# Kernel optimization log

Hardware: AMD Instinct MI355X
Metric: run time of the kernel (lower is better)

The kernel has to match this reference:

```python
import jax, jax.numpy as jnp
import numpy as np

WORD = 512
ED = 64


def setup_inputs() -> dict:
    key = jax.random.key(0)
    ks = jax.random.split(key, 7)
    x = jax.random.normal(ks[0], (4, 4096, WORD), dtype=jnp.float32)
    # Dense layer params (kernel + bias) for query/key/value projections
    s = 1.0 / np.sqrt(WORD)
    Wq = jax.random.normal(ks[1], (WORD, ED), dtype=jnp.float32) * s
    Wk = jax.random.normal(ks[2], (WORD, ED), dtype=jnp.float32) * s
    Wv = jax.random.normal(ks[3], (WORD, ED), dtype=jnp.float32) * s
    bq = jnp.zeros((ED,), dtype=jnp.float32)
    bk = jnp.zeros((ED,), dtype=jnp.float32)
    bv = jnp.zeros((ED,), dtype=jnp.float32)
    return {"x": x, "Wq": Wq, "bq": bq, "Wk": Wk, "bk": bk, "Wv": Wv, "bv": bv}


def reference(x, Wq, bq, Wk, bk, Wv, bv):
    # Q, K, V: [B, S, ED]
    Q = jnp.einsum('bsw,we->bse', x, Wq) + bq
    K = jnp.einsum('bsw,we->bse', x, Wk) + bk
    V = jnp.einsum('bsw,we->bse', x, Wv) + bv
    scale = 1.0 / jnp.sqrt(jnp.float32(ED))
    score = jnp.einsum('bqe,bke->bqk', Q, K) * scale  # [B, S, S]
    attn = jax.nn.softmax(score, axis=-1)
    Z = jnp.einsum('bqk,bke->bqe', attn, V)  # [B, S, ED]
    return Z
```

## Files before the change

### kernel.cpp

```cpp
#include <hip/hip_runtime.h>
#include <cstdint>


typedef __bf16 bf16x8 __attribute__((ext_vector_type(8)));
typedef float f32x4 __attribute__((ext_vector_type(4)));
typedef float f32x16 __attribute__((ext_vector_type(16)));
typedef int i32x2 __attribute__((ext_vector_type(2)));

#define SCALEQ 0.18033688011112042f

#define WT_OFF 0u
#define Q_OFF  262144u
#define KV_OFF 2359296u
#define L_OFF  6553600u
#define OP_OFF 7077888u

#if defined(__has_builtin)
#if __has_builtin(__builtin_amdgcn_permlane32_swap)
#define HAVE_PLSWAP 1
#endif
#if __has_builtin(__builtin_amdgcn_global_load_lds)
#define HAVE_GLL 1
#endif
#endif
#ifndef HAVE_PLSWAP
#define HAVE_PLSWAP 0
#endif
#ifndef HAVE_GLL
#define HAVE_GLL 0
#endif

__device__ __forceinline__ unsigned short bf16_1(float a) {
  unsigned ua = __builtin_bit_cast(unsigned, a);
  ua += 0x7FFFu + ((ua >> 16) & 1u);
  return (unsigned short)(ua >> 16);
}
__device__ __forceinline__ unsigned pk_bf16(float a, float b) {
  unsigned ua = __builtin_bit_cast(unsigned, a);
  unsigned ub = __builtin_bit_cast(unsigned, b);
  ua += 0x7FFFu + ((ua >> 16) & 1u);
  ub += 0x7FFFu + ((ub >> 16) & 1u);
  return (ua >> 16) | (ub & 0xFFFF0000u);
}
__device__ __forceinline__ unsigned pkru(float lo, float hi) {
  unsigned a = __builtin_bit_cast(unsigned, lo) + 0x8000u;
  unsigned b = __builtin_bit_cast(unsigned, hi) + 0x8000u;
  return __builtin_amdgcn_perm(b, a, 0x07060302u);
}
__device__ __forceinline__ void plswap(unsigned& x, unsigned& y, unsigned hl) {
#if HAVE_PLSWAP
  i32x2 r = __builtin_amdgcn_permlane32_swap((int)x, (int)y, false, false);
  x = (unsigned)r[0];
  y = (unsigned)r[1];
#else
  unsigned xs = (unsigned)__shfl_xor((int)x, 32);
  unsigned ys = (unsigned)__shfl_xor((int)y, 32);
  unsigned nx = hl ? ys : x;
  unsigned ny = hl ? y : xs;
  x = nx;
  y = ny;
#endif
}
#if HAVE_GLL
__device__ __forceinline__ void gll16(const void* g, void* l) {
  __builtin_amdgcn_global_load_lds(
      (const __attribute__((address_space(1))) void*)g,
      (__attribute__((address_space(3))) void*)l, 16, 0, 0);
}
#endif

__global__ __launch_bounds__(256) void prep_w(const float* __restrict__ Wq,
                                              const float* __restrict__ Wk,
                                              const float* __restrict__ Wv,
                                              unsigned short* __restrict__ wt2) {
  unsigned gtid = blockIdx.x * 256u + threadIdx.x;
  unsigned mat = gtid >> 15, rem = gtid & 32767u;
  const float* w = (mat == 0) ? Wq : (mat == 1) ? Wk : Wv;
  float v = w[rem];
  unsigned k = rem >> 6, n = rem & 63u;
  unsigned col = mat * 64u + n;
  unsigned ntg = col >> 4, l15c = col & 15u;
  unsigned kc = k >> 5, quad = (k >> 3) & 3u, j = k & 7u;
  wt2[((ntg * 16u + kc) * 64u + quad * 16u + l15c) * 8u + j] = bf16_1(v);
}

__global__ __launch_bounds__(256, 4) void qkv_proj(
    const float* __restrict__ x, const unsigned short* __restrict__ wt2,
    const float* __restrict__ bq, const float* __restrict__ bk,
    const float* __restrict__ bv, unsigned short* __restrict__ qws,
    unsigned short* __restrict__ kvws) {
  __shared__ __align__(16) char xs[16384];
  __shared__ float biasl[192];
  const unsigned t = threadIdx.x;
  const unsigned row0 = blockIdx.x * 16u;
  const unsigned w = t >> 6, lane = t & 63u, l15 = lane & 15u, quad = lane >> 4;

  if (t < 192u) {
    unsigned mat = t >> 6, n = t & 63u;
    biasl[t] = (mat == 0) ? bq[n] : (mat == 1) ? bk[n] : bv[n];
  }
#pragma unroll
  for (int i = 0; i < 8; i++) {
    unsigned idx4 = t + 256u * (unsigned)i;
    unsigned fidx = idx4 * 4u;
    unsigned row = fidx >> 9, k = fidx & 511u, g = k >> 3;
    float4 f = *(const float4*)(x + row0 * 512u + fidx);
    int2 v = make_int2(pkru(f.x, f.y), pkru(f.z, f.w));
    *(int2*)(xs + row * 1024u + ((g ^ (row & 7u)) << 4) + (k & 7u) * 2u) = v;
  }
  __syncthreads();

  f32x4 acc[3];
#pragma unroll
  for (int i = 0; i < 3; i++) acc[i] = {0.f, 0.f, 0.f, 0.f};
  const unsigned arow = l15;
  const unsigned short* wbase = wt2 + (w * 3u * 1024u + lane) * 8u;

  int4 cur[3], nxt[3];
#pragma unroll
  for (int nt = 0; nt < 3; nt++)
    cur[nt] = *(const int4*)(wbase + (unsigned)nt * 8192u);
  for (unsigned kc = 0; kc < 16u; kc++) {
    if (kc < 15u) {
#pragma unroll
      for (int nt = 0; nt < 3; nt++)
        nxt[nt] = *(const int4*)(wbase + ((unsigned)nt * 16u + kc + 1u) * 512u);
    }
    unsigned ag = kc * 4u + quad;
    int4 av = *(const int4*)(xs + arow * 1024u + ((ag ^ (arow & 7u)) << 4));
    bf16x8 a = __builtin_bit_cast(bf16x8, av);
#pragma unroll
    for (int nt = 0; nt < 3; nt++)
      acc[nt] = __builtin_amdgcn_mfma_f32_16x16x32_bf16(
          a, __builtin_bit_cast(bf16x8, cur[nt]), acc[nt], 0, 0, 0);
#pragma unroll
    for (int nt = 0; nt < 3; nt++) cur[nt] = nxt[nt];
  }
  unsigned sb = row0 + quad * 4u;
#pragma unroll
  for (int nt = 0; nt < 3; nt++) {
    unsigned col = w * 48u + (unsigned)nt * 16u + l15;
    unsigned mat = col >> 6, n = col & 63u;
    float bb = biasl[col];
    if (mat == 0) {
#pragma unroll
      for (int r = 0; r < 4; r++)
        qws[(sb + (unsigned)r) * 64u + n] = bf16_1((acc[nt][r] + bb) * SCALEQ);
    } else if (mat == 1) {
#pragma unroll
      for (int r = 0; r < 4; r++) {
        unsigned s = sb + (unsigned)r;
        unsigned bb2 = s >> 12, tile = (s & 4095u) >> 6, kap = s & 63u;
        kvws[(bb2 * 64u + tile) * 8192u + (n >> 3) * 512u + kap * 8u + (n & 7u)] =
            bf16_1(acc[nt][r] + bb);
      }
    } else {
      unsigned s = sb;
      unsigned bb2 = s >> 12, tile = (s & 4095u) >> 6;
      unsigned kg = (s & 63u) >> 3, j0 = s & 7u;
      int2 pv = make_int2(pk_bf16(acc[nt][0] + bb, acc[nt][1] + bb),
                          pk_bf16(acc[nt][2] + bb, acc[nt][3] + bb));
      *(int2*)(kvws + (bb2 * 64u + tile) * 8192u + (8u + kg) * 512u + n * 8u +
               j0) = pv;
    }
  }
}

__global__ __launch_bounds__(256, 3) void attn(
    const unsigned short* __restrict__ qws,
    const unsigned short* __restrict__ kvws, float* __restrict__ lws,
    unsigned short* __restrict__ opp) {
  __shared__ __align__(16) char sm[34816];
  const unsigned t = threadIdx.x;
  const unsigned w = t >> 6, lane = t & 63u, l31 = lane & 31u, hl = lane >> 5;
  const unsigned bid = blockIdx.x;
  const unsigned ks = bid >> 7;
  const unsigned b = (bid >> 5) & 3u;
  const unsigned qt = bid & 31u;
  const unsigned q0 = qt * 128u + w * 32u;
  const unsigned short* kvb = kvws + (b * 64u + ks * 8u) * 8192u + lane * 8u;

  bf16x8 qf[4];
#pragma unroll
  for (int kq = 0; kq < 4; kq++)
    qf[kq] = __builtin_bit_cast(
        bf16x8, *(const int4*)(qws + (b * 4096u + q0 + l31) * 64u +
                               (unsigned)kq * 16u + hl * 8u));
  f32x16 accO[2];
#pragma unroll
  for (int dh = 0; dh < 2; dh++)
#pragma unroll
    for (int r = 0; r < 16; r++) accO[dh][r] = 0.f;
  float lsum = 0.f;

#if HAVE_GLL
#define STAGE(kt_, bi_)                                                \
  {                                                                    \
    _Pragma("unroll") for (int i = 0; i < 4; i++) {                    \
      unsigned c = (unsigned)i * 4u + w;                               \
      gll16(kvb + (kt_)*8192u + c * 512u, sm + (bi_)*16384u + c * 1024u); \
    }                                                                  \
  }
  STAGE(0u, 0u);
  __syncthreads();
#else
  int4 stg[4];
#define LOADT(kt_)                                                         \
  {                                                                        \
    _Pragma("unroll") for (int i = 0; i < 4; i++) stg[i] =                 \
        *(const int4*)(kvb + (kt_)*8192u + ((unsigned)i * 4u + w) * 512u); \
  }
  LOADT(0u);
  {
#pragma unroll
    for (int i = 0; i < 4; i++)
      *(int4*)(sm + ((unsigned)i * 4u + w) * 1024u + lane * 16u) = stg[i];
  }
  __syncthreads();
#endif

  for (unsigned kt = 0; kt < 8u; kt++) {
    char* kb = sm + (kt & 1u) * 16384u;
    int4 kfr[8], vfr[8];
#pragma unroll
    for (int kq = 0; kq < 4; kq++)
#pragma unroll
      for (int kh = 0; kh < 2; kh++)
        kfr[kq * 2 + kh] = *(const int4*)(
            kb + (((unsigned)kq * 2u + hl) * 64u + (unsigned)kh * 32u + l31) * 16u);
#pragma unroll
    for (int kqg = 0; kqg < 4; kqg++)
#pragma unroll
      for (int dh = 0; dh < 2; dh++)
        vfr[kqg * 2 + dh] = *(const int4*)(
            kb + 8192u +
            (((unsigned)kqg * 2u + hl) * 64u + (unsigned)dh * 32u + l31) * 16u);
#if HAVE_GLL
    if (kt < 7u) STAGE(kt + 1u, (kt + 1u) & 1u);
#else
    if (kt < 7u) LOADT(kt + 1u);
#endif
#pragma unroll
    for (int kh = 0; kh < 2; kh++) {
      f32x16 z;
#pragma unroll
      for (int r = 0; r < 16; r++) z[r] = 0.f;
#pragma unroll
      for (int kq = 0; kq < 4; kq++)
        z = __builtin_amdgcn_mfma_f32_32x32x16_bf16(
            __builtin_bit_cast(bf16x8, kfr[kq * 2 + kh]), qf[kq], z, 0, 0, 0);
      float lp = 0.f;
#pragma unroll
      for (int r = 0; r < 16; r++) {
        z[r] = __builtin_amdgcn_exp2f(z[r]);
        lp += z[r];
      }
      lsum += lp;
      unsigned pk8[8];
#pragma unroll
      for (int c2 = 0; c2 < 4; c2++) {
        pk8[2 * c2] = pkru(z[4 * c2 + 0], z[4 * c2 + 1]);
        pk8[2 * c2 + 1] = pkru(z[4 * c2 + 2], z[4 * c2 + 3]);
      }
#pragma unroll
      for (int kqpl = 0; kqpl < 2; kqpl++) {
        unsigned a0 = pk8[4 * kqpl + 0], a1 = pk8[4 * kqpl + 1];
        unsigned b0 = pk8[4 * kqpl + 2], b1 = pk8[4 * kqpl + 3];
        plswap(a0, b0, hl);
        plswap(a1, b1, hl);
        int4 fr = make_int4((int)a0, (int)a1, (int)b0, (int)b1);
        bf16x8 pf = __builtin_bit_cast(bf16x8, fr);
        unsigned kqg = (unsigned)kh * 2u + (unsigned)kqpl;
#pragma unroll
        for (int dh = 0; dh < 2; dh++)
          accO[dh] = __builtin_amdgcn_mfma_f32_32x32x16_bf16(
              __builtin_bit_cast(bf16x8, vfr[kqg * 2u + (unsigned)dh]), pf,
              accO[dh], 0, 0, 0);
      }
    }
    __syncthreads();
#if !HAVE_GLL
    if (kt < 7u) {
#pragma unroll
      for (int i = 0; i < 4; i++)
        *(int4*)(sm + ((kt + 1u) & 1u) * 16384u +
                 ((unsigned)i * 4u + w) * 1024u + lane * 16u) = stg[i];
      __syncthreads();
    }
#endif
  }
  float lt = lsum + __shfl_xor(lsum, 32);
  if (hl == 0u) lws[ks * 16384u + b * 4096u + q0 + l31] = lt;
  float* sc = (float*)(sm + w * 8704u);
#pragma unroll
  for (int dh = 0; dh < 2; dh++)
#pragma unroll
    for (int r = 0; r < 16; r++) {
      unsigned d = (unsigned)dh * 32u + (unsigned)(r & 3) +
                   8u * (unsigned)(r >> 2) + 4u * hl;
      sc[l31 * 68u + d] = accO[dh][r];
    }
#pragma unroll
  for (int i = 0; i < 4; i++) {
    unsigned ql = (lane >> 3) + (unsigned)i * 8u;
    unsigned d0 = (lane & 7u) * 8u;
    float4 f0 = *(const float4*)(sc + ql * 68u + d0);
    float4 f1 = *(const float4*)(sc + ql * 68u + d0 + 4u);
    int4 pv = make_int4(pkru(f0.x, f0.y), pkru(f0.z, f0.w),
                        pkru(f1.x, f1.y), pkru(f1.z, f1.w));
    *(int4*)(opp + ks * 1048576u + (b * 4096u + q0 + ql) * 64u + d0) = pv;
  }
}

__global__ __launch_bounds__(256) void combine(const unsigned short* __restrict__ opp,
                                               const float* __restrict__ lws,
                                               float* __restrict__ out) {
#pragma unroll
  for (int ii = 0; ii < 2; ii++) {
    unsigned slot = blockIdx.x * 512u + threadIdx.x + 256u * (unsigned)ii;
    unsigned q = slot >> 4, c = (slot & 15u) * 4u;
    float l = 0.f;
#pragma unroll
    for (int s = 0; s < 8; s++) l += lws[(unsigned)s * 16384u + q];
    float inv = 1.0f / l;
    float4 r = make_float4(0.f, 0.f, 0.f, 0.f);
#pragma unroll
    for (int s = 0; s < 8; s++) {
      int2 pv = *(const int2*)(opp + (unsigned)s * 1048576u + q * 64u + c);
      r.x += __builtin_bit_cast(float, (unsigned)pv.x << 16);
      r.y += __builtin_bit_cast(float, (unsigned)pv.x & 0xFFFF0000u);
      r.z += __builtin_bit_cast(float, (unsigned)pv.y << 16);
      r.w += __builtin_bit_cast(float, (unsigned)pv.y & 0xFFFF0000u);
    }
    r.x *= inv; r.y *= inv; r.z *= inv; r.w *= inv;
    *(float4*)(out + q * 64u + c) = r;
  }
}

extern "C" void kernel_launch(void* const* d_in, const int* in_sizes, int n_in,
                              void* d_out, int out_size, void* d_ws,
                              size_t ws_size, hipStream_t stream) {
  const float* x = (const float*)d_in[0];
  const float* Wq = (const float*)d_in[1];
  const float* bq = (const float*)d_in[2];
  const float* Wk = (const float*)d_in[3];
  const float* bk = (const float*)d_in[4];
  const float* Wv = (const float*)d_in[5];
  const float* bv = (const float*)d_in[6];
  char* ws = (char*)d_ws;
  unsigned short* wt2 = (unsigned short*)(ws + WT_OFF);
  unsigned short* qb = (unsigned short*)(ws + Q_OFF);
  unsigned short* kvb = (unsigned short*)(ws + KV_OFF);
  float* lp = (float*)(ws + L_OFF);
  unsigned short* opp = (unsigned short*)(ws + OP_OFF);
  float* outp = (float*)d_out;

  prep_w<<<384, 256, 0, stream>>>(Wq, Wk, Wv, wt2);
  qkv_proj<<<1024, 256, 0, stream>>>(x, wt2, bq, bk, bv, qb, kvb);
  attn<<<1024, 256, 0, stream>>>(qb, kvb, lp, opp);
  combine<<<512, 256, 0, stream>>>(opp, lp, outp);
}
```

Before: 122.4 us.

## Rebalance attention key split to six chunks, double qkv rows per block, use cvt_pk_bf16

The attention kernel now splits keys into 6 uneven chunks (10-11 tiles each) instead of 8, giving 768 blocks rather than 1024 so the grid fits resident slots better and less partial output goes through combine. The QKV projection handles 32 rows per block so each weight fragment load feeds two MFMAs. Manual bf16 rounding is replaced with the hardware v_cvt_pk_bf16_f32 instruction, the exp-sum becomes a tree reduction, and s_setprio raises wave priority around the MFMA section. The trade-off is more work per attention block and uneven chunk sizes. It also uses more LDS in the projection kernel, which can lower occupancy.

```diff
diff --git a/kernel.cpp b/kernel.cpp
--- a/kernel.cpp
+++ b/kernel.cpp
@@ -35,17 +35,10 @@
   ua += 0x7FFFu + ((ua >> 16) & 1u);
   return (unsigned short)(ua >> 16);
 }
-__device__ __forceinline__ unsigned pk_bf16(float a, float b) {
-  unsigned ua = __builtin_bit_cast(unsigned, a);
-  unsigned ub = __builtin_bit_cast(unsigned, b);
-  ua += 0x7FFFu + ((ua >> 16) & 1u);
-  ub += 0x7FFFu + ((ub >> 16) & 1u);
-  return (ua >> 16) | (ub & 0xFFFF0000u);
-}
-__device__ __forceinline__ unsigned pkru(float lo, float hi) {
-  unsigned a = __builtin_bit_cast(unsigned, lo) + 0x8000u;
-  unsigned b = __builtin_bit_cast(unsigned, hi) + 0x8000u;
-  return __builtin_amdgcn_perm(b, a, 0x07060302u);
+__device__ __forceinline__ unsigned cvtpk(float lo, float hi) {
+  unsigned r;
+  asm("v_cvt_pk_bf16_f32 %0, %1, %2" : "=v"(r) : "v"(lo), "v"(hi));
+  return r;
 }
 __device__ __forceinline__ void plswap(unsigned& x, unsigned& y, unsigned hl) {
 #if HAVE_PLSWAP
@@ -89,10 +82,10 @@
     const float* __restrict__ bq, const float* __restrict__ bk,
     const float* __restrict__ bv, unsigned short* __restrict__ qws,
     unsigned short* __restrict__ kvws) {
-  __shared__ __align__(16) char xs[16384];
+  __shared__ __align__(16) char xs[32768];
   __shared__ float biasl[192];
   const unsigned t = threadIdx.x;
-  const unsigned row0 = blockIdx.x * 16u;
+  const unsigned row0 = blockIdx.x * 32u;
   const unsigned w = t >> 6, lane = t & 63u, l15 = lane & 15u, quad = lane >> 4;
 
   if (t < 192u) {
@@ -100,20 +93,21 @@
     biasl[t] = (mat == 0) ? bq[n] : (mat == 1) ? bk[n] : bv[n];
   }
 #pragma unroll
-  for (int i = 0; i < 8; i++) {
+  for (int i = 0; i < 16; i++) {
     unsigned idx4 = t + 256u * (unsigned)i;
     unsigned fidx = idx4 * 4u;
     unsigned row = fidx >> 9, k = fidx & 511u, g = k >> 3;
     float4 f = *(const float4*)(x + row0 * 512u + fidx);
-    int2 v = make_int2(pkru(f.x, f.y), pkru(f.z, f.w));
+    int2 v = make_int2((int)cvtpk(f.x, f.y), (int)cvtpk(f.z, f.w));
     *(int2*)(xs + row * 1024u + ((g ^ (row & 7u)) << 4) + (k & 7u) * 2u) = v;
   }
   __syncthreads();
 
-  f32x4 acc[3];
-#pragma unroll
-  for (int i = 0; i < 3; i++) acc[i] = {0.f, 0.f, 0.f, 0.f};
-  const unsigned arow = l15;
+  f32x4 acc[2][3];
+#pragma unroll
+  for (int rg = 0; rg < 2; rg++)
+#pragma unroll
+    for (int i = 0; i < 3; i++) acc[rg][i] = {0.f, 0.f, 0.f, 0.f};
   const unsigned short* wbase = wt2 + (w * 3u * 1024u + lane) * 8u;
 
   int4 cur[3], nxt[3];
@@ -127,41 +121,53 @@
         nxt[nt] = *(const int4*)(wbase + ((unsigned)nt * 16u + kc + 1u) * 512u);
     }
     unsigned ag = kc * 4u + quad;
-    int4 av = *(const int4*)(xs + arow * 1024u + ((ag ^ (arow & 7u)) << 4));
-    bf16x8 a = __builtin_bit_cast(bf16x8, av);
+    unsigned r1 = 16u + l15;
+    int4 av0 = *(const int4*)(xs + l15 * 1024u + ((ag ^ (l15 & 7u)) << 4));
+    int4 av1 = *(const int4*)(xs + r1 * 1024u + ((ag ^ (r1 & 7u)) << 4));
+    bf16x8 a0 = __builtin_bit_cast(bf16x8, av0);
+    bf16x8 a1 = __builtin_bit_cast(bf16x8, av1);
 #pragma unroll
     for (int nt = 0; nt < 3; nt++)
-      acc[nt] = __builtin_amdgcn_mfma_f32_16x16x32_bf16(
-          a, __builtin_bit_cast(bf16x8, cur[nt]), acc[nt], 0, 0, 0);
+      acc[0][nt] = __builtin_amdgcn_mfma_f32_16x16x32_bf16(
+          a0, __builtin_bit_cast(bf16x8, cur[nt]), acc[0][nt], 0, 0, 0);
+#pragma unroll
+    for (int nt = 0; nt < 3; nt++)
+      acc[1][nt] = __builtin_amdgcn_mfma_f32_16x16x32_bf16(
+          a1, __builtin_bit_cast(bf16x8, cur[nt]), acc[1][nt], 0, 0, 0);
 #pragma unroll
     for (int nt = 0; nt < 3; nt++) cur[nt] = nxt[nt];
   }
-  unsigned sb = row0 + quad * 4u;
-#pragma unroll
-  for (int nt = 0; nt < 3; nt++) {
-    unsigned col = w * 48u + (unsigned)nt * 16u + l15;
-    unsigned mat = col >> 6, n = col & 63u;
-    float bb = biasl[col];
-    if (mat == 0) {
-#pragma unroll
-      for (int r = 0; r < 4; r++)
-        qws[(sb + (unsigned)r) * 64u + n] = bf16_1((acc[nt][r] + bb) * SCALEQ);
-    } else if (mat == 1) {
-#pragma unroll
-      for (int r = 0; r < 4; r++) {
-        unsigned s = sb + (unsigned)r;
-        unsigned bb2 = s >> 12, tile = (s & 4095u) >> 6, kap = s & 63u;
-        kvws[(bb2 * 64u + tile) * 8192u + (n >> 3) * 512u + kap * 8u + (n & 7u)] =
-            bf16_1(acc[nt][r] + bb);
+#pragma unroll
+  for (int rg = 0; rg < 2; rg++) {
+    unsigned sb = row0 + (unsigned)rg * 16u + quad * 4u;
+#pragma unroll
+    for (int nt = 0; nt < 3; nt++) {
+      unsigned col = w * 48u + (unsigned)nt * 16u + l15;
+      unsigned mat = col >> 6, n = col & 63u;
+      float bb = biasl[col];
+      if (mat == 0) {
+#pragma unroll
+        for (int r = 0; r < 4; r++)
+          qws[(sb + (unsigned)r) * 64u + n] =
+              bf16_1((acc[rg][nt][r] + bb) * SCALEQ);
+      } else if (mat == 1) {
+#pragma unroll
+        for (int r = 0; r < 4; r++) {
+          unsigned s = sb + (unsigned)r;
+          unsigned bb2 = s >> 12, tile = (s & 4095u) >> 6, kap = s & 63u;
+          kvws[(bb2 * 64u + tile) * 8192u + (n >> 3) * 512u + kap * 8u +
+               (n & 7u)] = bf16_1(acc[rg][nt][r] + bb);
+        }
+      } else {
+        unsigned s = sb;
+        unsigned bb2 = s >> 12, tile = (s & 4095u) >> 6;
+        unsigned kg = (s & 63u) >> 3, j0 = s & 7u;
+        int2 pv =
+            make_int2((int)cvtpk(acc[rg][nt][0] + bb, acc[rg][nt][1] + bb),
+                      (int)cvtpk(acc[rg][nt][2] + bb, acc[rg][nt][3] + bb));
+        *(int2*)(kvws + (bb2 * 64u + tile) * 8192u + (8u + kg) * 512u + n * 8u +
+                 j0) = pv;
       }
-    } else {
-      unsigned s = sb;
-      unsigned bb2 = s >> 12, tile = (s & 4095u) >> 6;
-      unsigned kg = (s & 63u) >> 3, j0 = s & 7u;
-      int2 pv = make_int2(pk_bf16(acc[nt][0] + bb, acc[nt][1] + bb),
-                          pk_bf16(acc[nt][2] + bb, acc[nt][3] + bb));
-      *(int2*)(kvws + (bb2 * 64u + tile) * 8192u + (8u + kg) * 512u + n * 8u +
-               j0) = pv;
     }
   }
 }
@@ -178,7 +184,9 @@
   const unsigned b = (bid >> 5) & 3u;
   const unsigned qt = bid & 31u;
   const unsigned q0 = qt * 128u + w * 32u;
-  const unsigned short* kvb = kvws + (b * 64u + ks * 8u) * 8192u + lane * 8u;
+  const unsigned tile0 = ks * 10u + (ks < 4u ? ks : 4u);
+  const unsigned ntl = (ks < 4u) ? 11u : 10u;
+  const unsigned short* kvb = kvws + (b * 64u + tile0) * 8192u + lane * 8u;
 
   bf16x8 qf[4];
 #pragma unroll
@@ -219,7 +227,7 @@
   __syncthreads();
 #endif
 
-  for (unsigned kt = 0; kt < 8u; kt++) {
+  for (unsigned kt = 0; kt < ntl; kt++) {
     char* kb = sm + (kt & 1u) * 16384u;
     int4 kfr[8], vfr[8];
 #pragma unroll
@@ -236,10 +244,11 @@
             kb + 8192u +
             (((unsigned)kqg * 2u + hl) * 64u + (unsigned)dh * 32u + l31) * 16u);
 #if HAVE_GLL
-    if (kt < 7u) STAGE(kt + 1u, (kt + 1u) & 1u);
+    if (kt + 1u < ntl) STAGE(kt + 1u, (kt + 1u) & 1u);
 #else
-    if (kt < 7u) LOADT(kt + 1u);
-#endif
+    if (kt + 1u < ntl) LOADT(kt + 1u);
+#endif
+    __builtin_amdgcn_s_setprio(1);
 #pragma unroll
     for (int kh = 0; kh < 2; kh++) {
       f32x16 z;
@@ -249,18 +258,18 @@
       for (int kq = 0; kq < 4; kq++)
         z = __builtin_amdgcn_mfma_f32_32x32x16_bf16(
             __builtin_bit_cast(bf16x8, kfr[kq * 2 + kh]), qf[kq], z, 0, 0, 0);
-      float lp = 0.f;
-#pragma unroll
-      for (int r = 0; r < 16; r++) {
-        z[r] = __builtin_amdgcn_exp2f(z[r]);
-        lp += z[r];
-      }
-      lsum += lp;
+#pragma unroll
+      for (int r = 0; r < 16; r++) z[r] = __builtin_amdgcn_exp2f(z[r]);
+      float s0 = (z[0] + z[1]) + (z[2] + z[3]);
+      float s1 = (z[4] + z[5]) + (z[6] + z[7]);
+      float s2 = (z[8] + z[9]) + (z[10] + z[11]);
+      float s3 = (z[12] + z[13]) + (z[14] + z[15]);
+      lsum += (s0 + s1) + (s2 + s3);
       unsigned pk8[8];
 #pragma unroll
       for (int c2 = 0; c2 < 4; c2++) {
-        pk8[2 * c2] = pkru(z[4 * c2 + 0], z[4 * c2 + 1]);
-        pk8[2 * c2 + 1] = pkru(z[4 * c2 + 2], z[4 * c2 + 3]);
+        pk8[2 * c2] = cvtpk(z[4 * c2 + 0], z[4 * c2 + 1]);
+        pk8[2 * c2 + 1] = cvtpk(z[4 * c2 + 2], z[4 * c2 + 3]);
       }
 #pragma unroll
       for (int kqpl = 0; kqpl < 2; kqpl++) {
@@ -278,9 +287,10 @@
               accO[dh], 0, 0, 0);
       }
     }
+    __builtin_amdgcn_s_setprio(0);
     __syncthreads();
 #if !HAVE_GLL
-    if (kt < 7u) {
+    if (kt + 1u < ntl) {
 #pragma unroll
       for (int i = 0; i < 4; i++)
         *(int4*)(sm + ((kt + 1u) & 1u) * 16384u +
@@ -306,8 +316,8 @@
     unsigned d0 = (lane & 7u) * 8u;
     float4 f0 = *(const float4*)(sc + ql * 68u + d0);
     float4 f1 = *(const float4*)(sc + ql * 68u + d0 + 4u);
-    int4 pv = make_int4(pkru(f0.x, f0.y), pkru(f0.z, f0.w),
-                        pkru(f1.x, f1.y), pkru(f1.z, f1.w));
+    int4 pv = make_int4((int)cvtpk(f0.x, f0.y), (int)cvtpk(f0.z, f0.w),
+                        (int)cvtpk(f1.x, f1.y), (int)cvtpk(f1.z, f1.w));
     *(int4*)(opp + ks * 1048576u + (b * 4096u + q0 + ql) * 64u + d0) = pv;
   }
 }
@@ -321,11 +331,11 @@
     unsigned q = slot >> 4, c = (slot & 15u) * 4u;
     float l = 0.f;
 #pragma unroll
-    for (int s = 0; s < 8; s++) l += lws[(unsigned)s * 16384u + q];
+    for (int s = 0; s < 6; s++) l += lws[(unsigned)s * 16384u + q];
     float inv = 1.0f / l;
     float4 r = make_float4(0.f, 0.f, 0.f, 0.f);
 #pragma unroll
-    for (int s = 0; s < 8; s++) {
+    for (int s = 0; s < 6; s++) {
       int2 pv = *(const int2*)(opp + (unsigned)s * 1048576u + q * 64u + c);
       r.x += __builtin_bit_cast(float, (unsigned)pv.x << 16);
       r.y += __builtin_bit_cast(float, (unsigned)pv.x & 0xFFFF0000u);
@@ -356,7 +366,7 @@
   float* outp = (float*)d_out;
 
   prep_w<<<384, 256, 0, stream>>>(Wq, Wk, Wv, wt2);
-  qkv_proj<<<1024, 256, 0, stream>>>(x, wt2, bq, bk, bv, qb, kvb);
-  attn<<<1024, 256, 0, stream>>>(qb, kvb, lp, opp);
+  qkv_proj<<<512, 256, 0, stream>>>(x, wt2, bq, bk, bv, qb, kvb);
+  attn<<<768, 256, 0, stream>>>(qb, kvb, lp, opp);
   combine<<<512, 256, 0, stream>>>(opp, lp, outp);
 }
```

Result: faster. 117.1 us (-4.3%).
